# Optimization experiments

Hardware: AMD Instinct MI355X
Metric: run time of the kernel (lower is better)

Reference implementation:

```python
import jax, jax.numpy as jnp
import numpy as np
from jax import lax

KH = KW = 3
DIL = 4
D = DIL * (KH - 1) + 1  # dilated (effective) kernel extent = 9
PAD = 4
STRIDE = 1


def setup_inputs() -> dict:
    key = jax.random.key(0)
    k1, k2, k3, k4 = jax.random.split(key, 4)
    Cin, Cout, B, H, W = 128, 128, 16, 112, 112
    fan_in = Cin * KH * KW
    x = jax.random.normal(k1, (B, Cin, H, W), dtype=jnp.float32)
    weight = jax.random.normal(k2, (Cout, Cin, KH, KW), dtype=jnp.float32) / np.sqrt(fan_in)
    # learnable positions: offsets of each kernel point inside the dilated kernel
    P = jax.random.normal(k3, (2, Cout, Cin, KH, KW), dtype=jnp.float32) * (DIL / 2.0)
    bias = jax.random.normal(k4, (Cout,), dtype=jnp.float32) * 0.01
    return {"x": x, "weight": weight, "P": P, "bias": bias}


def _construct_kernel(weight, P):
    # Place each kernel point at its (learnable) continuous position inside the
    # D x D dilated kernel via bilinear interpolation (DCLS construction).
    O, C, kh, kw = weight.shape
    base_h = jnp.arange(kh, dtype=weight.dtype) * DIL  # regular dilated grid
    base_w = jnp.arange(kw, dtype=weight.dtype) * DIL
    p_h = jnp.clip(base_h[None, None, :, None] + P[0], 0.0, D - 1)  # (O,C,kh,kw)
    p_w = jnp.clip(base_w[None, None, None, :] + P[1], 0.0, D - 1)
    fh = jnp.floor(p_h)
    fw = jnp.floor(p_w)
    rh = p_h - fh  # fractional residuals -> bilinear weights
    rw = p_w - fw
    ih = fh.astype(jnp.int32)
    iw = fw.astype(jnp.int32)
    ih1 = jnp.minimum(ih + 1, D - 1)
    iw1 = jnp.minimum(iw + 1, D - 1)
    o = jnp.arange(O)[:, None, None, None]
    c = jnp.arange(C)[None, :, None, None]
    K = jnp.zeros((O, C, D, D), dtype=weight.dtype)
    K = K.at[o, c, ih, iw].add(weight * (1 - rh) * (1 - rw))
    K = K.at[o, c, ih1, iw].add(weight * rh * (1 - rw))
    K = K.at[o, c, ih, iw1].add(weight * (1 - rh) * rw)
    K = K.at[o, c, ih1, iw1].add(weight * rh * rw)
    return K


def reference(x, weight, P, bias):
    K = _construct_kernel(weight, P)  # (Cout, Cin, D, D)
    out = lax.conv_general_dilated(
        x, K,
        window_strides=(STRIDE, STRIDE),
        padding=[(PAD, PAD), (PAD, PAD)],
        dimension_numbers=("NCHW", "OIHW", "NCHW"),
        feature_group_count=1,
    )
    return out + bias[None, :, None, None]
```

## Files before the change

### kernel.cpp

```cpp
#include <hip/hip_runtime.h>
#include <hip/hip_bf16.h>
#include <stdint.h>


typedef __attribute__((ext_vector_type(8))) short short8;
typedef __attribute__((ext_vector_type(16))) float f32x16;

__device__ inline unsigned short f2bf(float f) {
    union { float f; unsigned int u; } v; v.f = f;
    unsigned int u = v.u;
    return (unsigned short)((u + 0x7FFFu + ((u >> 16) & 1u)) >> 16);
}

__global__ void build_K(const float* __restrict__ weight,
                        const float* __restrict__ P,
                        unsigned short* __restrict__ Kws) {
    __shared__ float sacc[128 * 81];
    int tid = threadIdx.x;
    int o = blockIdx.x;
    int c = tid;
    float* a = &sacc[c * 81];
    for (int i = 0; i < 81; ++i) a[i] = 0.0f;
    int base = (o * 128 + c) * 9;
    #pragma unroll
    for (int kh = 0; kh < 3; ++kh) {
        #pragma unroll
        for (int kw = 0; kw < 3; ++kw) {
            int kk = kh * 3 + kw;
            float w  = weight[base + kk];
            float p0 = P[base + kk];
            float p1 = P[128 * 128 * 9 + base + kk];
            float ph = fminf(fmaxf((float)(kh * 4) + p0, 0.0f), 8.0f);
            float pw = fminf(fmaxf((float)(kw * 4) + p1, 0.0f), 8.0f);
            float fh = floorf(ph), fw = floorf(pw);
            float rh = ph - fh, rw = pw - fw;
            int ih = (int)fh, iw = (int)fw;
            int ih1 = min(ih + 1, 8), iw1 = min(iw + 1, 8);
            a[ih  * 9 + iw ] += w * (1.0f - rh) * (1.0f - rw);
            a[ih1 * 9 + iw ] += w * rh * (1.0f - rw);
            a[ih  * 9 + iw1] += w * (1.0f - rh) * rw;
            a[ih1 * 9 + iw1] += w * rh * rw;
        }
    }
    __syncthreads();
    for (int u = tid; u < 1296; u += 128) {
        int tap = u >> 4;
        int rem = u & 15;
        int chunk = rem >> 1, half = rem & 1;
        int c0 = chunk * 16 + half * 8;
        short8 v;
        #pragma unroll
        for (int j = 0; j < 8; ++j)
            v[j] = (short)f2bf(sacc[(c0 + j) * 81 + tap]);
        *(short8*)(Kws + ((tap * 8 + chunk) * 2 + half) * 1024 + o * 8) = v;
    }
}

__global__ __launch_bounds__(256, 2)
void dcls_conv(const float* __restrict__ x,
               const unsigned short* __restrict__ Kws,
               const float* __restrict__ bias,
               float* __restrict__ out) {
    __shared__ __align__(16) char sX[18432];

    int bid = blockIdx.x;
    int b   = bid / 49;
    int rem = bid % 49;
    int ty  = rem / 7, tx = rem % 7;
    int y0  = ty * 16, x0 = tx * 16;

    int tid  = threadIdx.x;
    int lane = tid & 63;
    int wave = tid >> 6;
    int mgrp = wave >> 1;
    int ngrp = wave & 1;
    int half = lane >> 5;
    int l31  = lane & 31;
    int lrow = (lane >> 4) & 1;
    int lcol = lane & 15;

    f32x16 acc[2][4];
    #pragma unroll
    for (int i = 0; i < 2; ++i)
        #pragma unroll
        for (int j = 0; j < 4; ++j)
            #pragma unroll
            for (int k = 0; k < 16; ++k) acc[i][j][k] = 0.0f;

    int preAu[2];
    #pragma unroll
    for (int i = 0; i < 2; ++i)
        preAu[i] = half * 128 + ((mgrp * 2 + i) * 32 + l31);
    int preB[4];
    #pragma unroll
    for (int j = 0; j < 4; ++j)
        preB[j] = (2 * (ngrp * 4 + j) + lrow) * 768 + half * 384 + lcol * 16;

    const char* Kb = (const char*)Kws;

    for (int cc = 0; cc < 8; ++cc) {
        __syncthreads();
        {
            int cbase = cc * 16;
            #pragma unroll
            for (int it = 0; it < 5; ++it) {
                int u = tid + it * 256;
                if (u < 1152) {
                    int r  = u / 48;
                    int rr = u % 48;
                    int hf = rr / 24;
                    int co = rr % 24;
                    int h = y0 - 4 + r;
                    int w = x0 - 4 + co;
                    bool ok = (h >= 0) & (h < 112) & (w >= 0) & (w < 112);
                    const float* xp = x + (((b * 128 + cbase + hf * 8) * 112 + h) * 112 + w);
                    short8 v;
                    #pragma unroll
                    for (int j = 0; j < 8; ++j) {
                        float f = ok ? xp[j * 112 * 112] : 0.0f;
                        v[j] = (short)f2bf(f);
                    }
                    *(short8*)(sX + u * 16) = v;
                }
            }
        }
        __syncthreads();
        for (int tg = 0; tg < 9; ++tg) {
            #pragma unroll
            for (int t = 0; t < 9; ++t) {
                int tap = tg * 9 + t;
                const short8* kp =
                    (const short8*)(Kb + ((size_t)(tap * 8 + cc) << 12));
                short8 af[2];
                #pragma unroll
                for (int i = 0; i < 2; ++i)
                    af[i] = kp[preAu[i]];
                short8 bfr[4];
                int tapoff = tg * 768 + t * 16;
                #pragma unroll
                for (int j = 0; j < 4; ++j)
                    bfr[j] = *(const short8*)(sX + preB[j] + tapoff);
                #pragma unroll
                for (int i = 0; i < 2; ++i)
                    #pragma unroll
                    for (int j = 0; j < 4; ++j)
                        acc[i][j] = __builtin_amdgcn_mfma_f32_32x32x16_bf16(
                            af[i], bfr[j], acc[i][j], 0, 0, 0);
            }
        }
    }

    #pragma unroll
    for (int i = 0; i < 2; ++i) {
        int ob = (mgrp * 2 + i) * 32;
        #pragma unroll
        for (int r = 0; r < 16; ++r) {
            int o = ob + (r & 3) + 8 * (r >> 2) + 4 * half;
            float bv = bias[o];
            #pragma unroll
            for (int j = 0; j < 4; ++j) {
                int nt  = ngrp * 4 + j;
                int row = y0 + 2 * nt + lrow;
                int col = x0 + lcol;
                out[((b * 128 + o) * 112 + row) * 112 + col] = acc[i][j][r] + bv;
            }
        }
    }
}

extern "C" void kernel_launch(void* const* d_in, const int* in_sizes, int n_in,
                              void* d_out, int out_size, void* d_ws, size_t ws_size,
                              hipStream_t stream) {
    const float* x      = (const float*)d_in[0];
    const float* weight = (const float*)d_in[1];
    const float* P      = (const float*)d_in[2];
    const float* bias   = (const float*)d_in[3];
    float* out = (float*)d_out;
    unsigned short* Kws = (unsigned short*)d_ws;

    build_K<<<128, 128, 0, stream>>>(weight, P, Kws);
    dcls_conv<<<784, 256, 0, stream>>>(x, Kws, bias, out);
}
```

Baseline: 706.0 us.

## Remap waves to cover all Cout and double-buffer kernel-weight register loads

Changes the per-wave tile from 2x4 MFMA tiles (half of Cout, half of pixels) to 4x2 tiles (all 128 output channels, a quarter of the pixel rows). Global loads of the next tap's weight fragments are issued one tap ahead into a second register buffer, so their latency overlaps the current tap's MFMAs. Each wave now loads more weight data from global/L2 and fewer activation fragments from LDS. The extra double-buffered registers may raise register pressure at two blocks per SM.

```diff
diff --git a/kernel.cpp b/kernel.cpp
--- a/kernel.cpp
+++ b/kernel.cpp
@@ -72,31 +72,36 @@
     int tid  = threadIdx.x;
     int lane = tid & 63;
     int wave = tid >> 6;
-    int mgrp = wave >> 1;
-    int ngrp = wave & 1;
     int half = lane >> 5;
     int l31  = lane & 31;
     int lrow = (lane >> 4) & 1;
     int lcol = lane & 15;
 
-    f32x16 acc[2][4];
+    f32x16 acc[4][2];
     #pragma unroll
-    for (int i = 0; i < 2; ++i)
+    for (int i = 0; i < 4; ++i)
         #pragma unroll
-        for (int j = 0; j < 4; ++j)
+        for (int j = 0; j < 2; ++j)
             #pragma unroll
             for (int k = 0; k < 16; ++k) acc[i][j][k] = 0.0f;
 
-    int preAu[2];
+    int preAu[4];
     #pragma unroll
-    for (int i = 0; i < 2; ++i)
-        preAu[i] = half * 128 + ((mgrp * 2 + i) * 32 + l31);
-    int preB[4];
+    for (int i = 0; i < 4; ++i)
+        preAu[i] = half * 128 + (i * 32 + l31);
+    int preB[2];
     #pragma unroll
-    for (int j = 0; j < 4; ++j)
-        preB[j] = (2 * (ngrp * 4 + j) + lrow) * 768 + half * 384 + lcol * 16;
+    for (int j = 0; j < 2; ++j)
+        preB[j] = (2 * (wave * 2 + j) + lrow) * 768 + half * 384 + lcol * 16;
 
-    const char* Kb = (const char*)Kws;
+    const char* __restrict__ Kb = (const char*)Kws;
+
+    short8 af[2][4];
+    {
+        const short8* kp = (const short8*)Kb;
+        #pragma unroll
+        for (int i = 0; i < 4; ++i) af[0][i] = kp[preAu[i]];
+    }
 
     for (int cc = 0; cc < 8; ++cc) {
         __syncthreads();
@@ -129,37 +134,38 @@
             #pragma unroll
             for (int t = 0; t < 9; ++t) {
                 int tap = tg * 9 + t;
-                const short8* kp =
-                    (const short8*)(Kb + ((size_t)(tap * 8 + cc) << 12));
-                short8 af[2];
+                int cur = tap & 1;
+                int nslab = (tap == 80) ? (cc + 1) : ((tap + 1) * 8 + cc);
+                const short8* kn = (const short8*)(Kb + ((size_t)nslab << 12));
                 #pragma unroll
-                for (int i = 0; i < 2; ++i)
-                    af[i] = kp[preAu[i]];
-                short8 bfr[4];
+                for (int i = 0; i < 4; ++i) af[cur ^ 1][i] = kn[preAu[i]];
+                short8 bfr[2];
                 int tapoff = tg * 768 + t * 16;
                 #pragma unroll
-                for (int j = 0; j < 4; ++j)
+                for (int j = 0; j < 2; ++j)
                     bfr[j] = *(const short8*)(sX + preB[j] + tapoff);
                 #pragma unroll
-                for (int i = 0; i < 2; ++i)
+                for (int i = 0; i < 4; ++i)
                     #pragma unroll
-                    for (int j = 0; j < 4; ++j)
+                    for (int j = 0; j < 2; ++j)
                         acc[i][j] = __builtin_amdgcn_mfma_f32_32x32x16_bf16(
-                            af[i], bfr[j], acc[i][j], 0, 0, 0);
+                            af[cur][i], bfr[j], acc[i][j], 0, 0, 0);
             }
         }
+        #pragma unroll
+        for (int i = 0; i < 4; ++i) af[0][i] = af[1][i];
     }
 
     #pragma unroll
-    for (int i = 0; i < 2; ++i) {
-        int ob = (mgrp * 2 + i) * 32;
+    for (int i = 0; i < 4; ++i) {
+        int ob = i * 32;
         #pragma unroll
         for (int r = 0; r < 16; ++r) {
             int o = ob + (r & 3) + 8 * (r >> 2) + 4 * half;
             float bv = bias[o];
             #pragma unroll
-            for (int j = 0; j < 4; ++j) {
-                int nt  = ngrp * 4 + j;
+            for (int j = 0; j < 2; ++j) {
+                int nt  = wave * 2 + j;
                 int row = y0 + 2 * nt + lrow;
                 int col = x0 + lcol;
                 out[((b * 128 + o) * 112 + row) * 112 + col] = acc[i][j][r] + bv;
```

After: 903.2 us. +27.9%, slower.

## Stage weight tiles into LDS via async global_load_lds double buffering

Applied to the files above, without the earlier changes.

The weight (A) fragments were previously read directly from global memory inside the MFMA loop. They are now copied into two LDS buffers, three taps at a time, using async global-to-LDS loads. Waits on vmcnt plus barriers overlap the next group's copy with the current group's MFMAs. This hides global-load latency and cuts redundant per-wave global traffic. In exchange it adds 24KB of LDS, which may lower occupancy, plus extra barriers on every group of three taps.

```diff
diff --git a/kernel.cpp b/kernel.cpp
--- a/kernel.cpp
+++ b/kernel.cpp
@@ -56,12 +56,27 @@
     }
 }
 
+__device__ inline void dma3(const char* Kb, char* dst, int tapbase, int cc,
+                            int woff, int lane16) {
+    #pragma unroll
+    for (int j = 0; j < 3; ++j) {
+        const char* src = Kb + (((size_t)((tapbase + j) * 8 + cc)) << 12)
+                             + woff + lane16;
+        __builtin_amdgcn_global_load_lds(
+            (const __attribute__((address_space(1))) char*)src,
+            (__attribute__((address_space(3))) char*)(dst + j * 4096 + woff),
+            16, 0, 0);
+    }
+}
+
 __global__ __launch_bounds__(256, 2)
 void dcls_conv(const float* __restrict__ x,
                const unsigned short* __restrict__ Kws,
                const float* __restrict__ bias,
                float* __restrict__ out) {
     __shared__ __align__(16) char sX[18432];
+    __shared__ __align__(16) char sK0[12288];
+    __shared__ __align__(16) char sK1[12288];
 
     int bid = blockIdx.x;
     int b   = bid / 49;
@@ -78,6 +93,8 @@
     int l31  = lane & 31;
     int lrow = (lane >> 4) & 1;
     int lcol = lane & 15;
+    int woff = wave * 1024;
+    int lane16 = lane * 16;
 
     f32x16 acc[2][4];
     #pragma unroll
@@ -87,16 +104,16 @@
             #pragma unroll
             for (int k = 0; k < 16; ++k) acc[i][j][k] = 0.0f;
 
-    int preAu[2];
+    int preA[2];
     #pragma unroll
     for (int i = 0; i < 2; ++i)
-        preAu[i] = half * 128 + ((mgrp * 2 + i) * 32 + l31);
+        preA[i] = half * 2048 + ((mgrp * 2 + i) * 32 + l31) * 16;
     int preB[4];
     #pragma unroll
     for (int j = 0; j < 4; ++j)
         preB[j] = (2 * (ngrp * 4 + j) + lrow) * 768 + half * 384 + lcol * 16;
 
-    const char* Kb = (const char*)Kws;
+    const char* __restrict__ Kb = (const char*)Kws;
 
     for (int cc = 0; cc < 8; ++cc) {
         __syncthreads();
@@ -125,27 +142,40 @@
             }
         }
         __syncthreads();
-        for (int tg = 0; tg < 9; ++tg) {
-            #pragma unroll
-            for (int t = 0; t < 9; ++t) {
-                int tap = tg * 9 + t;
-                const short8* kp =
-                    (const short8*)(Kb + ((size_t)(tap * 8 + cc) << 12));
+
+        dma3(Kb, sK0, 0, cc, woff, lane16);
+        dma3(Kb, sK1, 3, cc, woff, lane16);
+
+        int tg = 0, t = 0;
+        for (int g = 0; g < 27; ++g) {
+            if (g < 26) {
+                asm volatile("s_waitcnt vmcnt(3)\n\ts_barrier" ::: "memory");
+            } else {
+                asm volatile("s_waitcnt vmcnt(0)\n\ts_barrier" ::: "memory");
+            }
+            char* buf = (g & 1) ? sK1 : sK0;
+            #pragma unroll
+            for (int j = 0; j < 3; ++j) {
+                int tapoff = tg * 768 + t * 16;
                 short8 af[2];
                 #pragma unroll
                 for (int i = 0; i < 2; ++i)
-                    af[i] = kp[preAu[i]];
+                    af[i] = *(const short8*)(buf + j * 4096 + preA[i]);
                 short8 bfr[4];
-                int tapoff = tg * 768 + t * 16;
                 #pragma unroll
-                for (int j = 0; j < 4; ++j)
-                    bfr[j] = *(const short8*)(sX + preB[j] + tapoff);
+                for (int jj = 0; jj < 4; ++jj)
+                    bfr[jj] = *(const short8*)(sX + preB[jj] + tapoff);
                 #pragma unroll
                 for (int i = 0; i < 2; ++i)
                     #pragma unroll
-                    for (int j = 0; j < 4; ++j)
-                        acc[i][j] = __builtin_amdgcn_mfma_f32_32x32x16_bf16(
-                            af[i], bfr[j], acc[i][j], 0, 0, 0);
+                    for (int jj = 0; jj < 4; ++jj)
+                        acc[i][jj] = __builtin_amdgcn_mfma_f32_32x32x16_bf16(
+                            af[i], bfr[jj], acc[i][jj], 0, 0, 0);
+                if (++t == 9) { t = 0; ++tg; }
+            }
+            if (g < 25) {
+                asm volatile("s_barrier" ::: "memory");
+                dma3(Kb, buf, (g + 2) * 3, cc, woff, lane16);
             }
         }
     }
```

Measured after the change: 612.3 us. -13.3%, faster.
